# Kernel optimization log

Hardware: AMD Instinct MI355X
Metric: run time of the kernel (lower is better)

The kernel has to match this reference:

```python
import jax, jax.numpy as jnp
from jax import lax
import numpy as np

T, N, H, E, R, L, VOCAB = 512, 200, 64, 16, 10, 2, 200


def setup_inputs() -> dict:
    key = jax.random.key(0)
    ks = jax.random.split(key, 20)
    s = 0.1
    return {
        "inputs": jax.random.normal(ks[0], (T, N), jnp.float32),
        "indices": jnp.arange(N, dtype=jnp.int64) % VOCAB,
        "embed_W": jax.random.normal(ks[1], (VOCAB, E), jnp.float32),
        "Wih0": jax.random.normal(ks[2], (4 * H, 1), jnp.float32) * s,
        "Whh0": jax.random.normal(ks[3], (4 * H, H), jnp.float32) * s,
        "bih0": jax.random.normal(ks[4], (4 * H,), jnp.float32) * s,
        "bhh0": jax.random.normal(ks[5], (4 * H,), jnp.float32) * s,
        "Wih1": jax.random.normal(ks[6], (4 * H, H), jnp.float32) * s,
        "Whh1": jax.random.normal(ks[7], (4 * H, H), jnp.float32) * s,
        "bih1": jax.random.normal(ks[8], (4 * H,), jnp.float32) * s,
        "bhh1": jax.random.normal(ks[9], (4 * H,), jnp.float32) * s,
        "Wm": jax.random.normal(ks[10], (H + E, 1), jnp.float32) * s,
        "bm": jnp.zeros((1,), jnp.float32),
        "Wv": jax.random.normal(ks[11], (H + E, R), jnp.float32) * s,
        "bv": jnp.zeros((R,), jnp.float32),
        "Wd": jax.random.normal(ks[12], (H + E, 1), jnp.float32) * s,
        "bd": jnp.zeros((1,), jnp.float32),
    }


def _cell(x, h, c, Wih, Whh, bih, bhh):
    # PyTorch LSTM cell, gate order i, f, g, o
    g = x @ Wih.T + bih + h @ Whh.T + bhh
    i, f, gg, o = jnp.split(g, 4, axis=-1)
    c_new = jax.nn.sigmoid(f) * c + jax.nn.sigmoid(i) * jnp.tanh(gg)
    h_new = jax.nn.sigmoid(o) * jnp.tanh(c_new)
    return h_new, c_new


def reference(inputs, indices, embed_W, Wih0, Whh0, bih0, bhh0,
              Wih1, Whh1, bih1, bhh1, Wm, bm, Wv, bv, Wd, bd):
    Tn, Nn = inputs.shape
    Hh = Whh0.shape[1]
    layers = [(Wih0, Whh0, bih0, bhh0), (Wih1, Whh1, bih1, bhh1)]
    h0 = jnp.zeros((len(layers), Nn, Hh), inputs.dtype)
    c0 = jnp.zeros_like(h0)

    def step(carry, x_t):
        h, c = carry              # [L, N, H]
        x = x_t[:, None]          # [N, 1] -- assets batched along batch dim
        hs, cs = [], []
        for l, (Wih, Whh, bih, bhh) in enumerate(layers):
            hn, cn = _cell(x, h[l], c[l], Wih, Whh, bih, bhh)
            hs.append(hn)
            cs.append(cn)
            x = hn
        return (jnp.stack(hs), jnp.stack(cs)), x

    _, out = lax.scan(step, (h0, c0), inputs)          # [T, N, H]
    emb = embed_W[indices]                              # [N, E]
    y = jnp.concatenate(
        [out, jnp.broadcast_to(emb[None], (Tn,) + emb.shape)], axis=-1
    )                                                   # [T, N, H+E]
    mu_t = y @ Wm + bm                                  # [T, N, 1]
    d_t = jax.nn.softplus(y @ Wd + bd)[..., 0]          # [T, N]
    v_t = y @ Wv + bv                                   # [T, N, R]
    eye = jnp.eye(Nn, dtype=inputs.dtype)
    cov_t = jnp.einsum('tnr,tmr->tnm', v_t, v_t) + d_t[:, :, None] * eye
    return mu_t, cov_t
```

## Files before the change

### kernel.cpp

```cpp
#include <hip/hip_runtime.h>
#include <hip/hip_bf16.h>
#include <math.h>

#define TT 512
#define NN 200
#define HH 64
#define EE 16
#define RR 10
#define MU_OFF 0
#define COV_OFF (TT*NN)
#define HBLK (NN*NN)
#define HPAD 68

__device__ __forceinline__ float sigmoidf_(float x) {
    return 1.0f / (1.0f + __expf(-x));
}
__device__ __forceinline__ float tanhf_(float x) {
    x = fminf(15.0f, fmaxf(-15.0f, x));
    float e = __expf(2.0f * x);
    return (e - 1.0f) / (e + 1.0f);
}

#define BAR() do { asm volatile("s_waitcnt lgkmcnt(0)" ::: "memory"); \
                   __builtin_amdgcn_s_barrier();                      \
                   asm volatile("" ::: "memory"); } while (0)

#define RQ(M) M(0) M(1) M(2) M(3) M(4) M(5) M(6) M(7) \
              M(8) M(9) M(10) M(11) M(12) M(13) M(14) M(15)

__global__
__attribute__((amdgpu_flat_work_group_size(512, 512), amdgpu_waves_per_eu(2, 2)))
void lstm_kernel(
    const float* __restrict__ inputs,
    const float* __restrict__ Wih0, const float* __restrict__ Whh0,
    const float* __restrict__ bih0, const float* __restrict__ bhh0,
    const float* __restrict__ Wih1, const float* __restrict__ Whh1,
    const float* __restrict__ bih1, const float* __restrict__ bhh1,
    float* __restrict__ out)
{
    const int n = blockIdx.x;
    const int tid = threadIdx.x;

    __shared__ float xs[TT];
    __shared__ float h0s[HH];
    __shared__ float h1s[HH];
    __shared__ float ga0[256];
    __shared__ float ga1[256];
    __shared__ float hist[64][HPAD];

    xs[tid] = inputs[tid * NN + n];
    if (tid < HH) { h0s[tid] = 0.0f; h1s[tid] = 0.0f; }

    float* covbase = out + COV_OFF + n * HH;

    if (tid < 256) {
        const float4* p0 = (const float4*)(Whh0 + tid * HH);
#define DECLA(q) float4 wA##q = p0[q];
        RQ(DECLA)
        const float wx = Wih0[tid];
        const float b0 = bih0[tid] + bhh0[tid];
        const bool  upd = (tid < HH);
        const int   gate = tid >> 6;
        float c0 = 0.0f;

        BAR();

        for (int t = 0; t <= TT; ++t) {
            if (t < TT) {
                float a0 = fmaf(wx, xs[t], b0), a1 = 0.f, a2 = 0.f, a3 = 0.f;
                const float4* h4 = (const float4*)h0s;
#define FMAA(q) { float4 h = h4[q];                  \
                  a0 = fmaf(wA##q.x, h.x, a0);       \
                  a1 = fmaf(wA##q.y, h.y, a1);       \
                  a2 = fmaf(wA##q.z, h.z, a2);       \
                  a3 = fmaf(wA##q.w, h.w, a3); }
                RQ(FMAA)
                float g = (a0 + a1) + (a2 + a3);
                ga0[tid] = (gate == 2) ? tanhf_(g) : sigmoidf_(g);
            }
            BAR();
            if (t < TT && upd) {
                float ia = ga0[tid], fa = ga0[tid + 64];
                float gg = ga0[tid + 128], oa = ga0[tid + 192];
                c0 = fmaf(fa, c0, ia * gg);
                h0s[tid] = oa * tanhf_(c0);
            }
            BAR();
            if ((t & 63) == 0 && t > 0) {
                const int s = tid >> 3;
                const int c = (tid & 7) * 8;
                float4 v0 = *(const float4*)&hist[s][c];
                float4 v1 = *(const float4*)&hist[s][c + 4];
                float* dst = covbase + (size_t)(t - 64 + s) * HBLK + c;
                ((float4*)dst)[0] = v0;
                ((float4*)dst)[1] = v1;
            }
        }
    } else {
        const int r = tid - 256;
        const float4* pi = (const float4*)(Wih1 + r * HH);
        const float4* ph = (const float4*)(Whh1 + r * HH);
#define DECLB(q) float4 wI##q = pi[q]; float4 wH##q = ph[q];
        RQ(DECLB)
        const float b1 = bih1[r] + bhh1[r];
        const bool  upd = (r < HH);
        const int   gate = r >> 6;
        float c1 = 0.0f;

        BAR();

        for (int t = 0; t <= TT; ++t) {
            if (t >= 1) {
                float a0 = b1, a1 = 0.f, a2 = 0.f, a3 = 0.f;
                float s0 = 0.f, s1 = 0.f, s2 = 0.f, s3 = 0.f;
                const float4* ha = (const float4*)h0s;
                const float4* hb = (const float4*)h1s;
#define FMAB(q) { float4 x = ha[q]; float4 y = hb[q]; \
                  a0 = fmaf(wI##q.x, x.x, a0);        \
                  a1 = fmaf(wI##q.y, x.y, a1);        \
                  a2 = fmaf(wI##q.z, x.z, a2);        \
                  a3 = fmaf(wI##q.w, x.w, a3);        \
                  s0 = fmaf(wH##q.x, y.x, s0);        \
                  s1 = fmaf(wH##q.y, y.y, s1);        \
                  s2 = fmaf(wH##q.z, y.z, s2);        \
                  s3 = fmaf(wH##q.w, y.w, s3); }
                RQ(FMAB)
                float g = ((a0 + a1) + (a2 + a3)) + ((s0 + s1) + (s2 + s3));
                ga1[r] = (gate == 2) ? tanhf_(g) : sigmoidf_(g);
            }
            BAR();
            if (t >= 1 && upd) {
                float ia = ga1[r], fa = ga1[r + 64];
                float gg = ga1[r + 128], oa = ga1[r + 192];
                c1 = fmaf(fa, c1, ia * gg);
                float h1 = oa * tanhf_(c1);
                h1s[r] = h1;
                hist[(t - 1) & 63][r] = h1;
            }
            BAR();
            if ((t & 63) == 0 && t > 0) {
                const int s = tid >> 3;
                const int c = (tid & 7) * 8;
                float4 v0 = *(const float4*)&hist[s][c];
                float4 v1 = *(const float4*)&hist[s][c + 4];
                float* dst = covbase + (size_t)(t - 64 + s) * HBLK + c;
                ((float4*)dst)[0] = v0;
                ((float4*)dst)[1] = v1;
            }
        }
    }
}

__global__ __launch_bounds__(256) void head_kernel(
    const float* __restrict__ embW, const int* __restrict__ indices,
    const float* __restrict__ Wm, const float* __restrict__ bm,
    const float* __restrict__ Wv, const float* __restrict__ bv,
    const float* __restrict__ Wd, const float* __restrict__ bd,
    float* __restrict__ out)
{
    const int t = blockIdx.x;
    const int tid = threadIdx.x;

    __shared__ float hs[NN * HH];
    __shared__ float embs[NN * EE];
    __shared__ float Wvs[(HH + EE) * RR];
    __shared__ float Wms[HH + EE];
    __shared__ float Wds[HH + EE];
    __shared__ float Vs[NN * (RR + 1)];
    __shared__ float dsh[NN];
    __shared__ float bvs[RR];

    const float* hsrc = out + COV_OFF + (size_t)t * HBLK;
    for (int i = tid; i < (NN * HH) / 4; i += 256)
        ((float4*)hs)[i] = ((const float4*)hsrc)[i];
    for (int i = tid; i < NN * EE; i += 256) {
        int n = i >> 4, e = i & 15;
        embs[i] = embW[indices[n] * EE + e];
    }
    for (int i = tid; i < (HH + EE) * RR; i += 256) Wvs[i] = Wv[i];
    if (tid < HH + EE) { Wms[tid] = Wm[tid]; Wds[tid] = Wd[tid]; }
    if (tid < RR) bvs[tid] = bv[tid];
    __syncthreads();

    for (int p = tid; p < NN * RR; p += 256) {
        int n = p / RR, r = p - n * RR;
        const float* hn = hs + n * HH;
        const float* en = embs + n * EE;
        float acc = bvs[r];
#pragma unroll 8
        for (int k = 0; k < HH; ++k) acc = fmaf(hn[k], Wvs[k * RR + r], acc);
#pragma unroll
        for (int k = 0; k < EE; ++k) acc = fmaf(en[k], Wvs[(HH + k) * RR + r], acc);
        Vs[n * (RR + 1) + r] = acc;
    }
    const float bmv = bm[0], bdv = bd[0];
    for (int n = tid; n < NN; n += 256) {
        const float* hn = hs + n * HH;
        const float* en = embs + n * EE;
        float am = bmv, ad = bdv;
#pragma unroll 8
        for (int k = 0; k < HH; ++k) {
            float h = hn[k];
            am = fmaf(h, Wms[k], am);
            ad = fmaf(h, Wds[k], ad);
        }
#pragma unroll
        for (int k = 0; k < EE; ++k) {
            float e = en[k];
            am = fmaf(e, Wms[HH + k], am);
            ad = fmaf(e, Wds[HH + k], ad);
        }
        out[MU_OFF + t * NN + n] = am;
        dsh[n] = (ad > 20.0f) ? ad : log1pf(__expf(ad));
    }
    __syncthreads();

    float* covp = out + COV_OFF + (size_t)t * HBLK;
    for (int p = tid; p < NN * NN; p += 256) {
        int n = p / NN, m = p - n * NN;
        const float* vn = Vs + n * (RR + 1);
        const float* vm = Vs + m * (RR + 1);
        float acc = (n == m) ? dsh[n] : 0.0f;
#pragma unroll
        for (int r = 0; r < RR; ++r) acc = fmaf(vn[r], vm[r], acc);
        covp[p] = acc;
    }
}

extern "C" void kernel_launch(void* const* d_in, const int* in_sizes, int n_in,
                              void* d_out, int out_size, void* d_ws, size_t ws_size,
                              hipStream_t stream) {
    const float* inputs  = (const float*)d_in[0];
    const int*   indices = (const int*)d_in[1];
    const float* embW    = (const float*)d_in[2];
    const float* Wih0    = (const float*)d_in[3];
    const float* Whh0    = (const float*)d_in[4];
    const float* bih0    = (const float*)d_in[5];
    const float* bhh0    = (const float*)d_in[6];
    const float* Wih1    = (const float*)d_in[7];
    const float* Whh1    = (const float*)d_in[8];
    const float* bih1    = (const float*)d_in[9];
    const float* bhh1    = (const float*)d_in[10];
    const float* Wm      = (const float*)d_in[11];
    const float* bm      = (const float*)d_in[12];
    const float* Wv      = (const float*)d_in[13];
    const float* bv      = (const float*)d_in[14];
    const float* Wd      = (const float*)d_in[15];
    const float* bd      = (const float*)d_in[16];
    float* out = (float*)d_out;

    lstm_kernel<<<NN, 512, 0, stream>>>(inputs, Wih0, Whh0, bih0, bhh0,
                                        Wih1, Whh1, bih1, bhh1, out);
    head_kernel<<<TT, 256, 0, stream>>>(embW, indices, Wm, bm, Wv, bv, Wd, bd, out);
}
```

Measured before the change: 475.8 us.

## Compute LSTM gate matvecs with bf16 MFMA instead of scalar FMA loops

```diff
diff --git a/kernel.cpp b/kernel.cpp
--- a/kernel.cpp
+++ b/kernel.cpp
@@ -12,6 +12,11 @@
 #define HBLK (NN*NN)
 #define HPAD 68
 
+typedef __bf16 bf16x8 __attribute__((ext_vector_type(8)));
+typedef float  f32x4  __attribute__((ext_vector_type(4)));
+
+#define MFMA(a,b,c) __builtin_amdgcn_mfma_f32_16x16x32_bf16(a, b, c, 0, 0, 0)
+
 __device__ __forceinline__ float sigmoidf_(float x) {
     return 1.0f / (1.0f + __expf(-x));
 }
@@ -20,13 +25,27 @@
     float e = __expf(2.0f * x);
     return (e - 1.0f) / (e + 1.0f);
 }
+__device__ __forceinline__ float act_(float g, bool is_tanh) {
+    float xx = is_tanh ? 2.0f * g : g;
+    float e = __expf(-xx);
+    float v = 1.0f / (1.0f + e);
+    return is_tanh ? fmaf(2.0f, v, -1.0f) : v;
+}
 
 #define BAR() do { asm volatile("s_waitcnt lgkmcnt(0)" ::: "memory"); \
                    __builtin_amdgcn_s_barrier();                      \
                    asm volatile("" ::: "memory"); } while (0)
 
-#define RQ(M) M(0) M(1) M(2) M(3) M(4) M(5) M(6) M(7) \
-              M(8) M(9) M(10) M(11) M(12) M(13) M(14) M(15)
+#define MT4(M) M(0) M(1) M(2) M(3)
+
+#define PACK8(dst, u0, u1) \
+    dst[0]=(__bf16)u0.x; dst[1]=(__bf16)u0.y; dst[2]=(__bf16)u0.z; dst[3]=(__bf16)u0.w; \
+    dst[4]=(__bf16)u1.x; dst[5]=(__bf16)u1.y; dst[6]=(__bf16)u1.z; dst[7]=(__bf16)u1.w;
+
+#define LDW(dst, p) { const float4* q4_ = (const float4*)(p); \
+    float4 u0_ = q4_[0], u1_ = q4_[1]; PACK8(dst, u0_, u1_) }
+
+#define PINF(v) asm volatile("" : "+v"(v))
 
 __global__
 __attribute__((amdgpu_flat_work_group_size(512, 512), amdgpu_waves_per_eu(2, 2)))
@@ -38,14 +57,16 @@
     const float* __restrict__ bih1, const float* __restrict__ bhh1,
     float* __restrict__ out)
 {
-    const int n = blockIdx.x;
-    const int tid = threadIdx.x;
+    const int n    = blockIdx.x;
+    const int tid  = threadIdx.x;
+    const int lane = tid & 63;
+    const int lm   = lane & 15;
+    const int kg   = lane >> 4;
+    const int wid  = tid >> 6;
 
     __shared__ float xs[TT];
-    __shared__ float h0s[HH];
-    __shared__ float h1s[HH];
-    __shared__ float ga0[256];
-    __shared__ float ga1[256];
+    __shared__ float h0s[HH], h1s[HH];
+    __shared__ float ga0[256], ga1[256];
     __shared__ float hist[64][HPAD];
 
     xs[tid] = inputs[tid * NN + n];
@@ -53,33 +74,47 @@
 
     float* covbase = out + COV_OFF + n * HH;
 
-    if (tid < 256) {
-        const float4* p0 = (const float4*)(Whh0 + tid * HH);
-#define DECLA(q) float4 wA##q = p0[q];
-        RQ(DECLA)
-        const float wx = Wih0[tid];
-        const float b0 = bih0[tid] + bhh0[tid];
-        const bool  upd = (tid < HH);
-        const int   gate = tid >> 6;
+    if (wid < 4) {
+        const int  RB   = wid * 64;
+        const bool is_t = (wid == 2);
+#define DECL0(mt) \
+        bf16x8 aA_##mt, aB_##mt; float4 wx_##mt, bb_##mt; \
+        { const float* pw_ = Whh0 + (size_t)(RB + mt*16 + lm) * HH + kg * 8; \
+          LDW(aA_##mt, pw_); LDW(aB_##mt, pw_ + 32); \
+          PINF(aA_##mt); PINF(aB_##mt); \
+          const int er_ = RB + mt*16 + kg*4; \
+          wx_##mt = *(const float4*)(Wih0 + er_); \
+          float4 b1_ = *(const float4*)(bih0 + er_); \
+          float4 b2_ = *(const float4*)(bhh0 + er_); \
+          bb_##mt.x = b1_.x + b2_.x; bb_##mt.y = b1_.y + b2_.y; \
+          bb_##mt.z = b1_.z + b2_.z; bb_##mt.w = b1_.w + b2_.w; }
+        MT4(DECL0)
         float c0 = 0.0f;
 
         BAR();
 
         for (int t = 0; t <= TT; ++t) {
             if (t < TT) {
-                float a0 = fmaf(wx, xs[t], b0), a1 = 0.f, a2 = 0.f, a3 = 0.f;
-                const float4* h4 = (const float4*)h0s;
-#define FMAA(q) { float4 h = h4[q];                  \
-                  a0 = fmaf(wA##q.x, h.x, a0);       \
-                  a1 = fmaf(wA##q.y, h.y, a1);       \
-                  a2 = fmaf(wA##q.z, h.z, a2);       \
-                  a3 = fmaf(wA##q.w, h.w, a3); }
-                RQ(FMAA)
-                float g = (a0 + a1) + (a2 + a3);
-                ga0[tid] = (gate == 2) ? tanhf_(g) : sigmoidf_(g);
+                const float x = xs[t];
+                bf16x8 B0, B1;
+                { const float4* p_ = (const float4*)(h0s + kg * 8);
+                  float4 u0_ = p_[0], u1_ = p_[1]; PACK8(B0, u0_, u1_) }
+                { const float4* p_ = (const float4*)(h0s + 32 + kg * 8);
+                  float4 u0_ = p_[0], u1_ = p_[1]; PACK8(B1, u0_, u1_) }
+#define MM0(mt) { f32x4 d_ = {0.f, 0.f, 0.f, 0.f}; \
+                d_ = MFMA(aA_##mt, B0, d_); \
+                d_ = MFMA(aB_##mt, B1, d_); \
+                float gx_ = act_(d_[0] + fmaf(wx_##mt.x, x, bb_##mt.x), is_t); \
+                float gy_ = act_(d_[1] + fmaf(wx_##mt.y, x, bb_##mt.y), is_t); \
+                float gz_ = act_(d_[2] + fmaf(wx_##mt.z, x, bb_##mt.z), is_t); \
+                float gw_ = act_(d_[3] + fmaf(wx_##mt.w, x, bb_##mt.w), is_t); \
+                if (lm == 0) { \
+                    float4 g_; g_.x = gx_; g_.y = gy_; g_.z = gz_; g_.w = gw_; \
+                    *(float4*)(ga0 + RB + mt*16 + kg*4) = g_; } }
+                MT4(MM0)
             }
             BAR();
-            if (t < TT && upd) {
+            if (t < TT && tid < HH) {
                 float ia = ga0[tid], fa = ga0[tid + 64];
                 float gg = ga0[tid + 128], oa = ga0[tid + 192];
                 c0 = fmaf(fa, c0, ia * gg);
@@ -87,63 +122,76 @@
             }
             BAR();
             if ((t & 63) == 0 && t > 0) {
-                const int s = tid >> 3;
-                const int c = (tid & 7) * 8;
-                float4 v0 = *(const float4*)&hist[s][c];
-                float4 v1 = *(const float4*)&hist[s][c + 4];
-                float* dst = covbase + (size_t)(t - 64 + s) * HBLK + c;
+                const int s  = tid >> 3;
+                const int cc = (tid & 7) * 8;
+                float4 v0 = *(const float4*)&hist[s][cc];
+                float4 v1 = *(const float4*)&hist[s][cc + 4];
+                float* dst = covbase + (size_t)(t - 64 + s) * HBLK + cc;
                 ((float4*)dst)[0] = v0;
                 ((float4*)dst)[1] = v1;
             }
         }
     } else {
-        const int r = tid - 256;
-        const float4* pi = (const float4*)(Wih1 + r * HH);
-        const float4* ph = (const float4*)(Whh1 + r * HH);
-#define DECLB(q) float4 wI##q = pi[q]; float4 wH##q = ph[q];
-        RQ(DECLB)
-        const float b1 = bih1[r] + bhh1[r];
-        const bool  upd = (r < HH);
-        const int   gate = r >> 6;
+        const int  RB   = (wid - 4) * 64;
+        const bool is_t = (wid == 6);
+#define DECL1(mt) \
+        bf16x8 aI0_##mt, aI1_##mt, aH0_##mt, aH1_##mt; float4 bb_##mt; \
+        { const size_t ro_ = (size_t)(RB + mt*16 + lm) * HH + kg * 8; \
+          LDW(aI0_##mt, Wih1 + ro_); LDW(aI1_##mt, Wih1 + ro_ + 32); \
+          LDW(aH0_##mt, Whh1 + ro_); LDW(aH1_##mt, Whh1 + ro_ + 32); \
+          PINF(aI0_##mt); PINF(aI1_##mt); PINF(aH0_##mt); PINF(aH1_##mt); \
+          const int er_ = RB + mt*16 + kg*4; \
+          float4 b1_ = *(const float4*)(bih1 + er_); \
+          float4 b2_ = *(const float4*)(bhh1 + er_); \
+          bb_##mt.x = b1_.x + b2_.x; bb_##mt.y = b1_.y + b2_.y; \
+          bb_##mt.z = b1_.z + b2_.z; bb_##mt.w = b1_.w + b2_.w; }
+        MT4(DECL1)
         float c1 = 0.0f;
 
         BAR();
 
         for (int t = 0; t <= TT; ++t) {
             if (t >= 1) {
-                float a0 = b1, a1 = 0.f, a2 = 0.f, a3 = 0.f;
-                float s0 = 0.f, s1 = 0.f, s2 = 0.f, s3 = 0.f;
-                const float4* ha = (const float4*)h0s;
-                const float4* hb = (const float4*)h1s;
-#define FMAB(q) { float4 x = ha[q]; float4 y = hb[q]; \
-                  a0 = fmaf(wI##q.x, x.x, a0);        \
-                  a1 = fmaf(wI##q.y, x.y, a1);        \
-                  a2 = fmaf(wI##q.z, x.z, a2);        \
-                  a3 = fmaf(wI##q.w, x.w, a3);        \
-                  s0 = fmaf(wH##q.x, y.x, s0);        \
-                  s1 = fmaf(wH##q.y, y.y, s1);        \
-                  s2 = fmaf(wH##q.z, y.z, s2);        \
-                  s3 = fmaf(wH##q.w, y.w, s3); }
-                RQ(FMAB)
-                float g = ((a0 + a1) + (a2 + a3)) + ((s0 + s1) + (s2 + s3));
-                ga1[r] = (gate == 2) ? tanhf_(g) : sigmoidf_(g);
+                bf16x8 B0, B1, B2, B3;
+                { const float4* p_ = (const float4*)(h0s + kg * 8);
+                  float4 u0_ = p_[0], u1_ = p_[1]; PACK8(B0, u0_, u1_) }
+                { const float4* p_ = (const float4*)(h0s + 32 + kg * 8);
+                  float4 u0_ = p_[0], u1_ = p_[1]; PACK8(B1, u0_, u1_) }
+                { const float4* p_ = (const float4*)(h1s + kg * 8);
+                  float4 u0_ = p_[0], u1_ = p_[1]; PACK8(B2, u0_, u1_) }
+                { const float4* p_ = (const float4*)(h1s + 32 + kg * 8);
+                  float4 u0_ = p_[0], u1_ = p_[1]; PACK8(B3, u0_, u1_) }
+#define MM1(mt) { f32x4 d_ = {0.f, 0.f, 0.f, 0.f}; \
+                d_ = MFMA(aI0_##mt, B0, d_); \
+                d_ = MFMA(aI1_##mt, B1, d_); \
+                d_ = MFMA(aH0_##mt, B2, d_); \
+                d_ = MFMA(aH1_##mt, B3, d_); \
+                float gx_ = act_(d_[0] + bb_##mt.x, is_t); \
+                float gy_ = act_(d_[1] + bb_##mt.y, is_t); \
+                float gz_ = act_(d_[2] + bb_##mt.z, is_t); \
+                float gw_ = act_(d_[3] + bb_##mt.w, is_t); \
+                if (lm == 0) { \
+                    float4 g_; g_.x = gx_; g_.y = gy_; g_.z = gz_; g_.w = gw_; \
+                    *(float4*)(ga1 + RB + mt*16 + kg*4) = g_; } }
+                MT4(MM1)
             }
             BAR();
-            if (t >= 1 && upd) {
-                float ia = ga1[r], fa = ga1[r + 64];
-                float gg = ga1[r + 128], oa = ga1[r + 192];
+            if (t >= 1 && tid >= 256 && tid < 256 + HH) {
+                const int j = tid - 256;
+                float ia = ga1[j], fa = ga1[j + 64];
+                float gg = ga1[j + 128], oa = ga1[j + 192];
                 c1 = fmaf(fa, c1, ia * gg);
                 float h1 = oa * tanhf_(c1);
-                h1s[r] = h1;
-                hist[(t - 1) & 63][r] = h1;
+                h1s[j] = h1;
+                hist[(t - 1) & 63][j] = h1;
             }
             BAR();
             if ((t & 63) == 0 && t > 0) {
-                const int s = tid >> 3;
-                const int c = (tid & 7) * 8;
-                float4 v0 = *(const float4*)&hist[s][c];
-                float4 v1 = *(const float4*)&hist[s][c + 4];
-                float* dst = covbase + (size_t)(t - 64 + s) * HBLK + c;
+                const int s  = tid >> 3;
+                const int cc = (tid & 7) * 8;
+                float4 v0 = *(const float4*)&hist[s][cc];
+                float4 v1 = *(const float4*)&hist[s][cc + 4];
+                float* dst = covbase + (size_t)(t - 64 + s) * HBLK + cc;
                 ((float4*)dst)[0] = v0;
                 ((float4*)dst)[1] = v1;
             }
```

Measured after the change: 986.4 us. 107% more time.

## Use bf16 dot2 matvec with LDS-staged weights and DPP quad reduction in LSTM

Applied to the files above, without the earlier changes.

```diff
diff --git a/kernel.cpp b/kernel.cpp
--- a/kernel.cpp
+++ b/kernel.cpp
@@ -20,13 +20,40 @@
     float e = __expf(2.0f * x);
     return (e - 1.0f) / (e + 1.0f);
 }
+__device__ __forceinline__ float act_(float g, bool is_tanh) {
+    float xx = is_tanh ? 2.0f * g : g;
+    float e = __expf(-xx);
+    float v = 1.0f / (1.0f + e);
+    return is_tanh ? fmaf(2.0f, v, -1.0f) : v;
+}
+
+__device__ __forceinline__ float dppxor1(float v) {
+    return __int_as_float(__builtin_amdgcn_mov_dpp(__float_as_int(v), 0xB1, 0xf, 0xf, true));
+}
+__device__ __forceinline__ float dppxor2(float v) {
+    return __int_as_float(__builtin_amdgcn_mov_dpp(__float_as_int(v), 0x4E, 0xf, 0xf, true));
+}
+
+__device__ __forceinline__ void dot2(float& acc, unsigned w, unsigned h) {
+    asm("v_dot2_f32_bf16 %0, %1, %2, %0" : "+v"(acc) : "v"(w), "v"(h));
+}
+
+__device__ __forceinline__ unsigned pk2(float a, float b) {
+    __bf16 x = (__bf16)a, y = (__bf16)b;
+    unsigned short ux = __builtin_bit_cast(unsigned short, x);
+    unsigned short uy = __builtin_bit_cast(unsigned short, y);
+    return (unsigned)ux | ((unsigned)uy << 16);
+}
+__device__ __forceinline__ unsigned short bfbits(float a) {
+    __bf16 x = (__bf16)a;
+    return __builtin_bit_cast(unsigned short, x);
+}
 
 #define BAR() do { asm volatile("s_waitcnt lgkmcnt(0)" ::: "memory"); \
                    __builtin_amdgcn_s_barrier();                      \
                    asm volatile("" ::: "memory"); } while (0)
 
-#define RQ(M) M(0) M(1) M(2) M(3) M(4) M(5) M(6) M(7) \
-              M(8) M(9) M(10) M(11) M(12) M(13) M(14) M(15)
+#define RM4(M) M(0) M(1) M(2) M(3)
 
 __global__
 __attribute__((amdgpu_flat_work_group_size(512, 512), amdgpu_waves_per_eu(2, 2)))
@@ -38,112 +65,161 @@
     const float* __restrict__ bih1, const float* __restrict__ bhh1,
     float* __restrict__ out)
 {
-    const int n = blockIdx.x;
+    const int n   = blockIdx.x;
     const int tid = threadIdx.x;
 
+    __shared__ uint4 wA[8 * 256];
+    __shared__ uint4 wB[16 * 256];
     __shared__ float xs[TT];
-    __shared__ float h0s[HH];
-    __shared__ float h1s[HH];
-    __shared__ float ga0[256];
-    __shared__ float ga1[256];
+    __shared__ __align__(16) unsigned short h0b[HH];
+    __shared__ __align__(16) unsigned short h1b[HH];
+    __shared__ float ga0[256], ga1[256];
     __shared__ float hist[64][HPAD];
 
     xs[tid] = inputs[tid * NN + n];
-    if (tid < HH) { h0s[tid] = 0.0f; h1s[tid] = 0.0f; }
+    if (tid < HH) { h0b[tid] = 0; h1b[tid] = 0; }
 
     float* covbase = out + COV_OFF + n * HH;
 
     if (tid < 256) {
-        const float4* p0 = (const float4*)(Whh0 + tid * HH);
-#define DECLA(q) float4 wA##q = p0[q];
-        RQ(DECLA)
+        const int b4 = tid & ~3;
+        const int qr = tid & 3;
+#define STGA(m) { const float* s_ = Whh0 + (b4 + m) * HH + qr * 16; \
+        uint4 p0_, p1_; \
+        p0_.x = pk2(s_[0], s_[1]);  p0_.y = pk2(s_[2], s_[3]); \
+        p0_.z = pk2(s_[4], s_[5]);  p0_.w = pk2(s_[6], s_[7]); \
+        p1_.x = pk2(s_[8], s_[9]);  p1_.y = pk2(s_[10], s_[11]); \
+        p1_.z = pk2(s_[12], s_[13]); p1_.w = pk2(s_[14], s_[15]); \
+        wA[(m * 2 + 0) * 256 + tid] = p0_; \
+        wA[(m * 2 + 1) * 256 + tid] = p1_; }
+        RM4(STGA)
         const float wx = Wih0[tid];
         const float b0 = bih0[tid] + bhh0[tid];
-        const bool  upd = (tid < HH);
-        const int   gate = tid >> 6;
+        const bool is_t = ((tid >> 6) == 2);
         float c0 = 0.0f;
 
         BAR();
 
         for (int t = 0; t <= TT; ++t) {
             if (t < TT) {
-                float a0 = fmaf(wx, xs[t], b0), a1 = 0.f, a2 = 0.f, a3 = 0.f;
-                const float4* h4 = (const float4*)h0s;
-#define FMAA(q) { float4 h = h4[q];                  \
-                  a0 = fmaf(wA##q.x, h.x, a0);       \
-                  a1 = fmaf(wA##q.y, h.y, a1);       \
-                  a2 = fmaf(wA##q.z, h.z, a2);       \
-                  a3 = fmaf(wA##q.w, h.w, a3); }
-                RQ(FMAA)
-                float g = (a0 + a1) + (a2 + a3);
-                ga0[tid] = (gate == 2) ? tanhf_(g) : sigmoidf_(g);
+                const float x = xs[t];
+                const uint4* hp = (const uint4*)(h0b + qr * 16);
+                uint4 ha = hp[0], hb = hp[1];
+                float acc0, acc1, acc2, acc3;
+#define MVA(m) { \
+                uint4 wa_ = wA[(m * 2 + 0) * 256 + tid]; \
+                uint4 wb_ = wA[(m * 2 + 1) * 256 + tid]; \
+                float a_ = 0.0f; \
+                dot2(a_, wa_.x, ha.x); dot2(a_, wa_.y, ha.y); \
+                dot2(a_, wa_.z, ha.z); dot2(a_, wa_.w, ha.w); \
+                dot2(a_, wb_.x, hb.x); dot2(a_, wb_.y, hb.y); \
+                dot2(a_, wb_.z, hb.z); dot2(a_, wb_.w, hb.w); \
+                acc##m = a_; }
+                RM4(MVA)
+                acc0 += dppxor1(acc0); acc0 += dppxor2(acc0);
+                acc1 += dppxor1(acc1); acc1 += dppxor2(acc1);
+                acc2 += dppxor1(acc2); acc2 += dppxor2(acc2);
+                acc3 += dppxor1(acc3); acc3 += dppxor2(acc3);
+                float g = (qr == 0) ? acc0 : (qr == 1) ? acc1 : (qr == 2) ? acc2 : acc3;
+                g += fmaf(wx, x, b0);
+                ga0[tid] = act_(g, is_t);
             }
             BAR();
-            if (t < TT && upd) {
+            if (t < TT && tid < HH) {
                 float ia = ga0[tid], fa = ga0[tid + 64];
                 float gg = ga0[tid + 128], oa = ga0[tid + 192];
                 c0 = fmaf(fa, c0, ia * gg);
-                h0s[tid] = oa * tanhf_(c0);
+                float h0n = oa * tanhf_(c0);
+                h0b[tid] = bfbits(h0n);
             }
             BAR();
             if ((t & 63) == 0 && t > 0) {
-                const int s = tid >> 3;
-                const int c = (tid & 7) * 8;
-                float4 v0 = *(const float4*)&hist[s][c];
-                float4 v1 = *(const float4*)&hist[s][c + 4];
-                float* dst = covbase + (size_t)(t - 64 + s) * HBLK + c;
+                const int s  = tid >> 3;
+                const int cc = (tid & 7) * 8;
+                float4 v0 = *(const float4*)&hist[s][cc];
+                float4 v1 = *(const float4*)&hist[s][cc + 4];
+                float* dst = covbase + (size_t)(t - 64 + s) * HBLK + cc;
                 ((float4*)dst)[0] = v0;
                 ((float4*)dst)[1] = v1;
             }
         }
     } else {
-        const int r = tid - 256;
-        const float4* pi = (const float4*)(Wih1 + r * HH);
-        const float4* ph = (const float4*)(Whh1 + r * HH);
-#define DECLB(q) float4 wI##q = pi[q]; float4 wH##q = ph[q];
-        RQ(DECLB)
+        const int r  = tid - 256;
+        const int b4 = r & ~3;
+        const int qr = r & 3;
+#define STGB(m) { \
+        const float* si_ = Wih1 + (b4 + m) * HH + qr * 16; \
+        const float* sh_ = Whh1 + (b4 + m) * HH + qr * 16; \
+        uint4 p0_, p1_, p2_, p3_; \
+        p0_.x = pk2(si_[0], si_[1]);  p0_.y = pk2(si_[2], si_[3]); \
+        p0_.z = pk2(si_[4], si_[5]);  p0_.w = pk2(si_[6], si_[7]); \
+        p1_.x = pk2(si_[8], si_[9]);  p1_.y = pk2(si_[10], si_[11]); \
+        p1_.z = pk2(si_[12], si_[13]); p1_.w = pk2(si_[14], si_[15]); \
+        p2_.x = pk2(sh_[0], sh_[1]);  p2_.y = pk2(sh_[2], sh_[3]); \
+        p2_.z = pk2(sh_[4], sh_[5]);  p2_.w = pk2(sh_[6], sh_[7]); \
+        p3_.x = pk2(sh_[8], sh_[9]);  p3_.y = pk2(sh_[10], sh_[11]); \
+        p3_.z = pk2(sh_[12], sh_[13]); p3_.w = pk2(sh_[14], sh_[15]); \
+        wB[(m * 4 + 0) * 256 + r] = p0_; \
+        wB[(m * 4 + 1) * 256 + r] = p1_; \
+        wB[(m * 4 + 2) * 256 + r] = p2_; \
+        wB[(m * 4 + 3) * 256 + r] = p3_; }
+        RM4(STGB)
         const float b1 = bih1[r] + bhh1[r];
-        const bool  upd = (r < HH);
-        const int   gate = r >> 6;
+        const bool is_t = ((r >> 6) == 2);
         float c1 = 0.0f;
 
         BAR();
 
         for (int t = 0; t <= TT; ++t) {
             if (t >= 1) {
-                float a0 = b1, a1 = 0.f, a2 = 0.f, a3 = 0.f;
-                float s0 = 0.f, s1 = 0.f, s2 = 0.f, s3 = 0.f;
-                const float4* ha = (const float4*)h0s;
-                const float4* hb = (const float4*)h1s;
-#define FMAB(q) { float4 x = ha[q]; float4 y = hb[q]; \
-                  a0 = fmaf(wI##q.x, x.x, a0);        \
-                  a1 = fmaf(wI##q.y, x.y, a1);        \
-                  a2 = fmaf(wI##q.z, x.z, a2);        \
-                  a3 = fmaf(wI##q.w, x.w, a3);        \
-                  s0 = fmaf(wH##q.x, y.x, s0);        \
-                  s1 = fmaf(wH##q.y, y.y, s1);        \
-                  s2 = fmaf(wH##q.z, y.z, s2);        \
-                  s3 = fmaf(wH##q.w, y.w, s3); }
-                RQ(FMAB)
-                float g = ((a0 + a1) + (a2 + a3)) + ((s0 + s1) + (s2 + s3));
-                ga1[r] = (gate == 2) ? tanhf_(g) : sigmoidf_(g);
+                int idx = r;
+                asm volatile("" : "+v"(idx));
+                const uint4* hp0 = (const uint4*)(h0b + qr * 16);
+                const uint4* hp1 = (const uint4*)(h1b + qr * 16);
+                uint4 ha0 = hp0[0], ha1 = hp0[1];
+                uint4 hb0 = hp1[0], hb1 = hp1[1];
+                float acc0, acc1, acc2, acc3;
+#define MVB(m) { \
+                uint4 wi0_ = wB[(m * 4 + 0) * 256 + idx]; \
+                uint4 wi1_ = wB[(m * 4 + 1) * 256 + idx]; \
+                uint4 wh0_ = wB[(m * 4 + 2) * 256 + idx]; \
+                uint4 wh1_ = wB[(m * 4 + 3) * 256 + idx]; \
+                float a_ = 0.0f; \
+                dot2(a_, wi0_.x, ha0.x); dot2(a_, wi0_.y, ha0.y); \
+                dot2(a_, wi0_.z, ha0.z); dot2(a_, wi0_.w, ha0.w); \
+                dot2(a_, wi1_.x, ha1.x); dot2(a_, wi1_.y, ha1.y); \
+                dot2(a_, wi1_.z, ha1.z); dot2(a_, wi1_.w, ha1.w); \
+                dot2(a_, wh0_.x, hb0.x); dot2(a_, wh0_.y, hb0.y); \
+                dot2(a_, wh0_.z, hb0.z); dot2(a_, wh0_.w, hb0.w); \
+                dot2(a_, wh1_.x, hb1.x); dot2(a_, wh1_.y, hb1.y); \
+                dot2(a_, wh1_.z, hb1.z); dot2(a_, wh1_.w, hb1.w); \
+                acc##m = a_; }
+                RM4(MVB)
+                acc0 += dppxor1(acc0); acc0 += dppxor2(acc0);
+                acc1 += dppxor1(acc1); acc1 += dppxor2(acc1);
+                acc2 += dppxor1(acc2); acc2 += dppxor2(acc2);
+                acc3 += dppxor1(acc3); acc3 += dppxor2(acc3);
+                float g = (qr == 0) ? acc0 : (qr == 1) ? acc1 : (qr == 2) ? acc2 : acc3;
+                g += b1;
+                ga1[r] = act_(g, is_t);
             }
             BAR();
-            if (t >= 1 && upd) {
-                float ia = ga1[r], fa = ga1[r + 64];
-                float gg = ga1[r + 128], oa = ga1[r + 192];
+            if (t >= 1 && tid < 256 + HH) {
+                const int j = tid - 256;
+                float ia = ga1[j], fa = ga1[j + 64];
+                float gg = ga1[j + 128], oa = ga1[j + 192];
                 c1 = fmaf(fa, c1, ia * gg);
                 float h1 = oa * tanhf_(c1);
-                h1s[r] = h1;
-                hist[(t - 1) & 63][r] = h1;
+                h1b[j] = bfbits(h1);
+                hist[(t - 1) & 63][j] = h1;
             }
             BAR();
             if ((t & 63) == 0 && t > 0) {
-                const int s = tid >> 3;
-                const int c = (tid & 7) * 8;
-                float4 v0 = *(const float4*)&hist[s][c];
-                float4 v1 = *(const float4*)&hist[s][c + 4];
-                float* dst = covbase + (size_t)(t - 64 + s) * HBLK + c;
+                const int s  = tid >> 3;
+                const int cc = (tid & 7) * 8;
+                float4 v0 = *(const float4*)&hist[s][cc];
+                float4 v1 = *(const float4*)&hist[s][cc + 4];
+                float* dst = covbase + (size_t)(t - 64 + s) * HBLK + cc;
                 ((float4*)dst)[0] = v0;
                 ((float4*)dst)[1] = v1;
             }
```

Result: faster. 454.8 us (-4.4%).
